# Performance work log

Measured on AMD Instinct MI355X. Metric: run time of the kernel, lower is better.

## Reference

```python
import jax, jax.numpy as jnp
import numpy as np

N = 100000      # nodes
E = 1600000     # edges (before self-loops)
IN = 256        # in_channels
HID = 16        # num_hid (per-head channels, layer 1)
HEADS = 4
OUT = 16        # out_channels (per-head channels, layer 2)
NEG_SLOPE = 0.2 # PyG GATConv default


def setup_inputs() -> dict:
    key = jax.random.key(0)
    ks = jax.random.split(key, 12)
    def glorot(k, shape, fan):
        return jax.random.normal(k, shape, jnp.float32) * (1.0 / np.sqrt(fan))
    x = jax.random.normal(ks[0], (N, IN), jnp.float32)
    edge_index = jax.random.randint(ks[1], (2, E), 0, N, dtype=jnp.int32)
    W1 = glorot(ks[2], (IN, HEADS * HID), IN)
    att_src1 = glorot(ks[3], (HEADS, HID), HID)
    att_dst1 = glorot(ks[4], (HEADS, HID), HID)
    b1 = jnp.zeros((HEADS * HID,), jnp.float32)
    W2 = glorot(ks[5], (HEADS * HID, HEADS * OUT), HEADS * HID)
    att_src2 = glorot(ks[6], (HEADS, OUT), OUT)
    att_dst2 = glorot(ks[7], (HEADS, OUT), OUT)
    b2 = jnp.zeros((HEADS * OUT,), jnp.float32)
    return {"x": x, "edge_index": edge_index, "W1": W1, "att_src1": att_src1,
            "att_dst1": att_dst1, "b1": b1, "W2": W2, "att_src2": att_src2,
            "att_dst2": att_dst2, "b2": b2}


def gat_conv(x, W, att_src, att_dst, bias, src, dst):
    # PyG GATConv (concat=True): h = xW per head; alpha via segment-softmax over dst.
    H, C = att_src.shape
    n = x.shape[0]
    h = (x @ W).reshape(n, H, C)                    # [N,H,C]
    a_s = jnp.sum(h * att_src, axis=-1)             # [N,H]
    a_d = jnp.sum(h * att_dst, axis=-1)             # [N,H]
    e = jax.nn.leaky_relu(a_s[src] + a_d[dst], NEG_SLOPE)  # [E',H]
    m = jax.lax.stop_gradient(jax.ops.segment_max(e, dst, num_segments=n))
    p = jnp.exp(e - m[dst])
    s = jax.ops.segment_sum(p, dst, num_segments=n)
    alpha = p / (s[dst] + 1e-16)                    # [E',H]
    msg = h[src] * alpha[:, :, None]                # [E',H,C] gathered messages
    out = jax.ops.segment_sum(msg, dst, num_segments=n)
    return out.reshape(n, H * C) + bias


def reference(x, edge_index, W1, att_src1, att_dst1, b1, W2, att_src2, att_dst2, b2):
    # add self loops (PyG GATConv default add_self_loops=True)
    loops = jnp.arange(N, dtype=edge_index.dtype)
    src = jnp.concatenate([edge_index[0], loops])
    dst = jnp.concatenate([edge_index[1], loops])
    h = jax.nn.relu(gat_conv(x, W1, att_src1, att_dst1, b1, src, dst))
    # dropout is identity in eval mode
    return gat_conv(h, W2, att_src2, att_dst2, b2, src, dst)
```

## Files before the change

### kernel.cpp

```cpp
#include <hip/hip_runtime.h>
#include <hip/hip_fp16.h>
#include <cstdint>


#define CH 4096
#define MAXB 512
#define SCAP 6144

using f16x8 = __attribute__((ext_vector_type(8))) _Float16;
using f32x4 = __attribute__((ext_vector_type(4))) float;

__device__ __forceinline__ float lrelu(float v) { return fmaxf(v, 0.2f * v); }

__global__ void ifill_kernel(int* __restrict__ p, int v, int n) {
  int i = blockIdx.x * blockDim.x + threadIdx.x;
  if (i < n) p[i] = v;
}

__global__ void wprep2_kernel(const float* __restrict__ W,
                              const float* __restrict__ as,
                              const float* __restrict__ ad,
                              ushort* __restrict__ WT, int K) {
  int i = blockIdx.x * 256 + threadIdx.x;
  if (i >= 80 * K) return;
  int c = i / K, k = i % K;
  float v = 0.f;
  if (c < 64) {
    v = W[k * 64 + c];
  } else if (c < 68) {
    int hd = c - 64;
    for (int j = 0; j < 16; ++j) v += W[k * 64 + hd * 16 + j] * as[hd * 16 + j];
  } else if (c < 72) {
    int hd = c - 68;
    for (int j = 0; j < 16; ++j) v += W[k * 64 + hd * 16 + j] * ad[hd * 16 + j];
  }
  WT[c * K + k] = __half_as_ushort(__float2half_rn(v));
}

__global__ __launch_bounds__(256) void bucket_hist(const int* __restrict__ edst,
                                                   int E, int nbuck,
                                                   int* __restrict__ bucket_cnt) {
  __shared__ int hist[MAXB];
  const int t = threadIdx.x;
  for (int j = t; j < MAXB; j += 256) hist[j] = 0;
  __syncthreads();
  const int base = blockIdx.x * CH;
#pragma unroll
  for (int k = 0; k < CH / 256; ++k) {
    int e = base + k * 256 + t;
    if (e < E) atomicAdd(&hist[edst[e] >> 8], 1);
  }
  __syncthreads();
  for (int j = t; j < nbuck; j += 256) {
    int c = hist[j];
    if (c) atomicAdd(&bucket_cnt[j], c);
  }
}

__global__ __launch_bounds__(512) void bucket_scan(const int* __restrict__ bucket_cnt,
                                                   int* __restrict__ bucket_base,
                                                   int* __restrict__ bucket_cursor,
                                                   int nbuck) {
  __shared__ int part[512];
  const int t = threadIdx.x;
  int v = (t < nbuck) ? bucket_cnt[t] : 0;
  part[t] = v;
  __syncthreads();
  for (int off = 1; off < 512; off <<= 1) {
    int u = (t >= off) ? part[t - off] : 0;
    __syncthreads();
    part[t] += u;
    __syncthreads();
  }
  int ex = part[t] - v;
  if (t <= nbuck) {
    int w = (t < nbuck) ? ex : part[nbuck - 1];
    bucket_base[t] = w;
    if (t < nbuck) bucket_cursor[t] = w;
  }
}

__global__ __launch_bounds__(256) void place_kernel(const int* __restrict__ esrc,
                                                    const int* __restrict__ edst,
                                                    int E, int nbuck,
                                                    int* __restrict__ bucket_cursor,
                                                    unsigned int* __restrict__ pairs) {
  __shared__ int hist[MAXB];
  __shared__ int gbase[MAXB];
  __shared__ int rcnt[MAXB];
  const int t = threadIdx.x;
  for (int j = t; j < MAXB; j += 256) { hist[j] = 0; rcnt[j] = 0; }
  __syncthreads();
  const int base = blockIdx.x * CH;
  int b_[CH / 256];
  unsigned int p_[CH / 256];
#pragma unroll
  for (int k = 0; k < CH / 256; ++k) {
    int e = base + k * 256 + t;
    if (e < E) {
      int d = edst[e];
      int s = esrc[e];
      b_[k] = d >> 8;
      p_[k] = ((unsigned int)s << 8) | (unsigned int)(d & 255);
      atomicAdd(&hist[b_[k]], 1);
    } else {
      b_[k] = -1;
    }
  }
  __syncthreads();
  for (int j = t; j < nbuck; j += 256) {
    int c = hist[j];
    gbase[j] = c ? atomicAdd(&bucket_cursor[j], c) : 0;
  }
  __syncthreads();
#pragma unroll
  for (int k = 0; k < CH / 256; ++k) {
    if (b_[k] >= 0) {
      int r = atomicAdd(&rcnt[b_[k]], 1);
      pairs[gbase[b_[k]] + r] = p_[k];
    }
  }
}

__global__ __launch_bounds__(256) void bucket_build(
    const unsigned int* __restrict__ pairs, const int* __restrict__ bucket_base,
    int* __restrict__ ccol, int* __restrict__ start, int* __restrict__ endp,
    int n) {
  __shared__ int cnt[256];
  __shared__ int ls[256];
  __shared__ int csave[256];
  __shared__ int part[256];
  __shared__ int sorted[SCAP];
  const int t = threadIdx.x;
  const int b = blockIdx.x;
  const int d0 = b << 8;
  const int DR = min(256, n - d0);
  const int in_base = bucket_base[b];
  const int nloc = bucket_base[b + 1] - in_base;
  const int out_base = in_base + d0;

  cnt[t] = (t < DR) ? 1 : 0;
  __syncthreads();
  for (int i = t; i < nloc; i += 256)
    atomicAdd(&cnt[pairs[in_base + i] & 255u], 1);
  __syncthreads();
  int c = cnt[t];
  csave[t] = c;
  part[t] = c;
  __syncthreads();
#pragma unroll
  for (int off = 1; off < 256; off <<= 1) {
    int u = (t >= off) ? part[t - off] : 0;
    __syncthreads();
    part[t] += u;
    __syncthreads();
  }
  ls[t] = part[t] - c;
  __syncthreads();
  if (t < DR) {
    int s = out_base + ls[t];
    start[d0 + t] = s;
    endp[d0 + t] = s + csave[t];
    sorted[ls[t]] = d0 + t;
    cnt[t] = 1;
  }
  __syncthreads();
  for (int i = t; i < nloc; i += 256) {
    unsigned int p = pairs[in_base + i];
    int j = (int)(p & 255u);
    int r = atomicAdd(&cnt[j], 1);
    int pos = ls[j] + r;
    if (pos < SCAP) sorted[pos] = (int)(p >> 8);
  }
  __syncthreads();
  int tot = nloc + DR;
  if (tot > SCAP) tot = SCAP;
  for (int i = t; i < tot; i += 256) ccol[out_base + i] = sorted[i];
}

template <int K, bool XHALF>
__global__ __launch_bounds__(256) void gemm_mfma(
    const void* __restrict__ xin, const ushort* __restrict__ wt,
    __half* __restrict__ h, float* __restrict__ as_, float* __restrict__ ad_,
    int n) {
  __shared__ _Float16 hs[64 * 88];
  __shared__ float att[64 * 12];
  const int tid = threadIdx.x;
  const int w = tid >> 6;
  const int lane = tid & 63;
  const int lr = lane & 15;
  const int kg = lane >> 4;
  const int row0 = blockIdx.x * 64;

  int rr = row0 + w * 16 + lr;
  if (rr > n - 1) rr = n - 1;

  constexpr int NS = K / 32;
  const ushort* wbase = wt + lr * K + kg * 8;

  f16x8 af[NS];
  if constexpr (!XHALF) {
    float4 av[NS][2];
    const float* xp = (const float*)xin + (long long)rr * K + kg * 8;
#pragma unroll
    for (int s = 0; s < NS; ++s) {
      av[s][0] = *(const float4*)(xp + s * 32);
      av[s][1] = *(const float4*)(xp + s * 32 + 4);
    }
#pragma unroll
    for (int s = 0; s < NS; ++s) {
      af[s][0] = (_Float16)av[s][0].x; af[s][1] = (_Float16)av[s][0].y;
      af[s][2] = (_Float16)av[s][0].z; af[s][3] = (_Float16)av[s][0].w;
      af[s][4] = (_Float16)av[s][1].x; af[s][5] = (_Float16)av[s][1].y;
      af[s][6] = (_Float16)av[s][1].z; af[s][7] = (_Float16)av[s][1].w;
    }
  } else {
    const ushort* xp = (const ushort*)xin + (long long)rr * K + kg * 8;
#pragma unroll
    for (int s = 0; s < NS; ++s)
      af[s] = *(const f16x8*)(xp + s * 32);
  }

  f32x4 acc[5] = {};
#pragma unroll
  for (int s = 0; s < NS; ++s) {
#pragma unroll
    for (int ct = 0; ct < 5; ++ct) {
      f16x8 b = *(const f16x8*)(wbase + ct * 16 * K + s * 32);
      acc[ct] = __builtin_amdgcn_mfma_f32_16x16x32_f16(af[s], b, acc[ct], 0, 0, 0);
    }
  }

  const int orow = w * 16 + kg * 4;
#pragma unroll
  for (int ct = 0; ct < 4; ++ct)
#pragma unroll
    for (int r = 0; r < 4; ++r)
      hs[(orow + r) * 88 + ct * 16 + lr] = (_Float16)acc[ct][r];
  if (lr < 8) {
#pragma unroll
    for (int r = 0; r < 4; ++r)
      att[(orow + r) * 12 + lr] = acc[4][r];
  }
  __syncthreads();

#pragma unroll
  for (int j = 0; j < 2; ++j) {
    int s = tid + j * 256;
    int row = s >> 3, seg = s & 7;
    if (row0 + row < n)
      *(uint4*)(h + (long long)(row0 + row) * 64 + seg * 8) =
          *(const uint4*)&hs[row * 88 + seg * 8];
  }
  if (tid < 64) {
    if (row0 + tid < n)
      *(float4*)(as_ + (long long)(row0 + tid) * 4) = *(const float4*)&att[tid * 12];
  } else if (tid < 128) {
    int t2 = tid - 64;
    if (row0 + t2 < n)
      *(float4*)(ad_ + (long long)(row0 + t2) * 4) = *(const float4*)&att[t2 * 12 + 4];
  }
}

__global__ __launch_bounds__(256) void node_agg_kernel(
    const int* __restrict__ ccol, const int* __restrict__ start,
    const int* __restrict__ endp,
    const float* __restrict__ as_, const float* __restrict__ ad_,
    const __half2* __restrict__ h2, const float* __restrict__ bias,
    float* __restrict__ fout, __half2* __restrict__ hout, int n, int mode) {
  const int node = blockIdx.x * 8 + (threadIdx.x >> 5);
  if (node >= n) return;
  const int hl = threadIdx.x & 31;
  const int hh = hl >> 3;
  const float adv = ad_[node * 4 + hh];
  const int s0i = start[node];
  const int d = endp[node] - s0i;
  const int* cp = ccol + s0i;
  float ax = 0.f, ay = 0.f, den = 0.f;
  int i = 0;
  for (; i + 4 <= d; i += 4) {
    int s0 = cp[i], s1 = cp[i + 1], s2 = cp[i + 2], s3 = cp[i + 3];
    float p0 = __expf(lrelu(as_[s0 * 4 + hh] + adv));
    float p1 = __expf(lrelu(as_[s1 * 4 + hh] + adv));
    float p2 = __expf(lrelu(as_[s2 * 4 + hh] + adv));
    float p3 = __expf(lrelu(as_[s3 * 4 + hh] + adv));
    float2 h0 = __half22float2(h2[s0 * 32 + hl]);
    float2 h1 = __half22float2(h2[s1 * 32 + hl]);
    float2 h2v = __half22float2(h2[s2 * 32 + hl]);
    float2 h3 = __half22float2(h2[s3 * 32 + hl]);
    den += (p0 + p1) + (p2 + p3);
    ax = fmaf(p0, h0.x, ax); ay = fmaf(p0, h0.y, ay);
    ax = fmaf(p1, h1.x, ax); ay = fmaf(p1, h1.y, ay);
    ax = fmaf(p2, h2v.x, ax); ay = fmaf(p2, h2v.y, ay);
    ax = fmaf(p3, h3.x, ax); ay = fmaf(p3, h3.y, ay);
  }
  for (; i < d; ++i) {
    int s0 = cp[i];
    float p0 = __expf(lrelu(as_[s0 * 4 + hh] + adv));
    float2 h0 = __half22float2(h2[s0 * 32 + hl]);
    den += p0;
    ax = fmaf(p0, h0.x, ax); ay = fmaf(p0, h0.y, ay);
  }
  const float inv = 1.0f / (den + 1e-16f);
  float vx = ax * inv + bias[hl * 2];
  float vy = ay * inv + bias[hl * 2 + 1];
  if (mode == 1) {
    vx = fmaxf(vx, 0.f);
    vy = fmaxf(vy, 0.f);
    hout[node * 32 + hl] = __floats2half2_rn(vx, vy);
  } else {
    *(float2*)(fout + node * 64 + hl * 2) = make_float2(vx, vy);
  }
}

extern "C" void kernel_launch(void* const* d_in, const int* in_sizes, int n_in,
                              void* d_out, int out_size, void* d_ws, size_t ws_size,
                              hipStream_t stream) {
  const float* x = (const float*)d_in[0];
  const int* ei = (const int*)d_in[1];
  const float* W1 = (const float*)d_in[2];
  const float* att_s1 = (const float*)d_in[3];
  const float* att_d1 = (const float*)d_in[4];
  const float* b1 = (const float*)d_in[5];
  const float* W2 = (const float*)d_in[6];
  const float* att_s2 = (const float*)d_in[7];
  const float* att_d2 = (const float*)d_in[8];
  const float* b2 = (const float*)d_in[9];

  const int n = in_sizes[0] / 256;
  const int E = in_sizes[1] / 2;
  const int* esrc = ei;
  const int* edst = ei + E;
  const int nbuck = (n + 255) >> 8;

  float* wsf = (float*)d_ws;
  __half* hbuf = (__half*)wsf;
  float* xbuf = wsf + (long long)n * 64;
  float* as_ = xbuf + (long long)n * 64;
  float* ad_ = as_ + (long long)n * 4;
  int* bucket_cnt = (int*)(ad_ + (long long)n * 4);
  int* bucket_base = bucket_cnt + MAXB;
  int* bucket_cursor = bucket_base + MAXB + 1;
  int* start = bucket_cursor + MAXB;
  int* endp = start + n;
  unsigned int* pairs = (unsigned int*)(endp + n);
  int* ccol = (int*)(pairs + E);
  ushort* wt1 = (ushort*)(((uintptr_t)(ccol + E + n) + 15) & ~(uintptr_t)15);
  ushort* wt2 = wt1 + 80 * 256;
  float* out = (float*)d_out;

  const int ebk = (E + CH - 1) / CH;
  const int gb = (n + 63) / 64;
  const int nb = (n + 7) / 8;

  wprep2_kernel<<<(80 * 256 + 255) / 256, 256, 0, stream>>>(W1, att_s1, att_d1, wt1, 256);
  wprep2_kernel<<<(80 * 64 + 255) / 256, 256, 0, stream>>>(W2, att_s2, att_d2, wt2, 64);

  ifill_kernel<<<(MAXB + 255) / 256, 256, 0, stream>>>(bucket_cnt, 0, MAXB);
  bucket_hist<<<ebk, 256, 0, stream>>>(edst, E, nbuck, bucket_cnt);
  bucket_scan<<<1, 512, 0, stream>>>(bucket_cnt, bucket_base, bucket_cursor, nbuck);
  place_kernel<<<ebk, 256, 0, stream>>>(esrc, edst, E, nbuck, bucket_cursor, pairs);
  bucket_build<<<nbuck, 256, 0, stream>>>(pairs, bucket_base, ccol, start, endp, n);

  gemm_mfma<256, false><<<gb, 256, 0, stream>>>(x, wt1, hbuf, as_, ad_, n);
  node_agg_kernel<<<nb, 256, 0, stream>>>(ccol, start, endp, as_, ad_,
                                          (const __half2*)hbuf, b1,
                                          nullptr, (__half2*)xbuf, n, 1);

  gemm_mfma<64, true><<<gb, 256, 0, stream>>>(xbuf, wt2, hbuf, as_, ad_, n);
  node_agg_kernel<<<nb, 256, 0, stream>>>(ccol, start, endp, as_, ad_,
                                          (const __half2*)hbuf, b2,
                                          out, nullptr, n, 0);
}
```

Before: 226.8 us.

## Fuse GEMM and aggregation stages into persistent kernel with grid barriers

Replaces the two GEMM and two aggregation launches with a single persistent kernel of 256 blocks that loops over tiles and node groups. The stages are separated by atomic-counter grid barriers, and the counters are zeroed by an extra fill launch. This removes inter-kernel launch gaps and tail effects. In exchange, the gather-heavy aggregation runs with far fewer resident blocks, which may reduce latency hiding, and the barrier relies on all blocks being co-resident.

```diff
diff --git a/kernel.cpp b/kernel.cpp
--- a/kernel.cpp
+++ b/kernel.cpp
@@ -6,6 +6,7 @@
 #define CH 4096
 #define MAXB 512
 #define SCAP 6144
+#define GRID_FUSED 256
 
 using f16x8 = __attribute__((ext_vector_type(8))) _Float16;
 using f32x4 = __attribute__((ext_vector_type(4))) float;
@@ -178,139 +179,176 @@
   for (int i = t; i < tot; i += 256) ccol[out_base + i] = sorted[i];
 }
 
+__device__ __forceinline__ void gsync(int* bar, int idx, int goal) {
+  __threadfence();
+  __syncthreads();
+  if (threadIdx.x == 0) {
+    atomicAdd(&bar[idx], 1);
+    while (atomicAdd(&bar[idx], 0) < goal) __builtin_amdgcn_s_sleep(2);
+  }
+  __syncthreads();
+  __threadfence();
+}
+
 template <int K, bool XHALF>
-__global__ __launch_bounds__(256) void gemm_mfma(
+__device__ __forceinline__ void gemm_phase(
     const void* __restrict__ xin, const ushort* __restrict__ wt,
     __half* __restrict__ h, float* __restrict__ as_, float* __restrict__ ad_,
-    int n) {
-  __shared__ _Float16 hs[64 * 88];
-  __shared__ float att[64 * 12];
+    int n, int ntiles, _Float16* hs, float* att) {
   const int tid = threadIdx.x;
   const int w = tid >> 6;
   const int lane = tid & 63;
   const int lr = lane & 15;
   const int kg = lane >> 4;
-  const int row0 = blockIdx.x * 64;
-
-  int rr = row0 + w * 16 + lr;
-  if (rr > n - 1) rr = n - 1;
-
   constexpr int NS = K / 32;
   const ushort* wbase = wt + lr * K + kg * 8;
 
-  f16x8 af[NS];
-  if constexpr (!XHALF) {
-    float4 av[NS][2];
-    const float* xp = (const float*)xin + (long long)rr * K + kg * 8;
-#pragma unroll
-    for (int s = 0; s < NS; ++s) {
-      av[s][0] = *(const float4*)(xp + s * 32);
-      av[s][1] = *(const float4*)(xp + s * 32 + 4);
-    }
-#pragma unroll
-    for (int s = 0; s < NS; ++s) {
-      af[s][0] = (_Float16)av[s][0].x; af[s][1] = (_Float16)av[s][0].y;
-      af[s][2] = (_Float16)av[s][0].z; af[s][3] = (_Float16)av[s][0].w;
-      af[s][4] = (_Float16)av[s][1].x; af[s][5] = (_Float16)av[s][1].y;
-      af[s][6] = (_Float16)av[s][1].z; af[s][7] = (_Float16)av[s][1].w;
-    }
-  } else {
-    const ushort* xp = (const ushort*)xin + (long long)rr * K + kg * 8;
+  for (int tile = blockIdx.x; tile < ntiles; tile += gridDim.x) {
+    const int row0 = tile * 64;
+    int rr = row0 + w * 16 + lr;
+    if (rr > n - 1) rr = n - 1;
+
+    f16x8 af[NS];
+    if constexpr (!XHALF) {
+      float4 av[NS][2];
+      const float* xp = (const float*)xin + (long long)rr * K + kg * 8;
+#pragma unroll
+      for (int s = 0; s < NS; ++s) {
+        av[s][0] = *(const float4*)(xp + s * 32);
+        av[s][1] = *(const float4*)(xp + s * 32 + 4);
+      }
+#pragma unroll
+      for (int s = 0; s < NS; ++s) {
+        af[s][0] = (_Float16)av[s][0].x; af[s][1] = (_Float16)av[s][0].y;
+        af[s][2] = (_Float16)av[s][0].z; af[s][3] = (_Float16)av[s][0].w;
+        af[s][4] = (_Float16)av[s][1].x; af[s][5] = (_Float16)av[s][1].y;
+        af[s][6] = (_Float16)av[s][1].z; af[s][7] = (_Float16)av[s][1].w;
+      }
+    } else {
+      const ushort* xp = (const ushort*)xin + (long long)rr * K + kg * 8;
+#pragma unroll
+      for (int s = 0; s < NS; ++s)
+        af[s] = *(const f16x8*)(xp + s * 32);
+    }
+
+    f32x4 acc[5] = {};
 #pragma unroll
     for (int s = 0; s < NS; ++s)
-      af[s] = *(const f16x8*)(xp + s * 32);
-  }
-
-  f32x4 acc[5] = {};
-#pragma unroll
-  for (int s = 0; s < NS; ++s) {
-#pragma unroll
-    for (int ct = 0; ct < 5; ++ct) {
-      f16x8 b = *(const f16x8*)(wbase + ct * 16 * K + s * 32);
-      acc[ct] = __builtin_amdgcn_mfma_f32_16x16x32_f16(af[s], b, acc[ct], 0, 0, 0);
-    }
-  }
-
-  const int orow = w * 16 + kg * 4;
-#pragma unroll
-  for (int ct = 0; ct < 4; ++ct)
-#pragma unroll
-    for (int r = 0; r < 4; ++r)
-      hs[(orow + r) * 88 + ct * 16 + lr] = (_Float16)acc[ct][r];
-  if (lr < 8) {
-#pragma unroll
-    for (int r = 0; r < 4; ++r)
-      att[(orow + r) * 12 + lr] = acc[4][r];
-  }
-  __syncthreads();
-
-#pragma unroll
-  for (int j = 0; j < 2; ++j) {
-    int s = tid + j * 256;
-    int row = s >> 3, seg = s & 7;
-    if (row0 + row < n)
-      *(uint4*)(h + (long long)(row0 + row) * 64 + seg * 8) =
-          *(const uint4*)&hs[row * 88 + seg * 8];
-  }
-  if (tid < 64) {
-    if (row0 + tid < n)
-      *(float4*)(as_ + (long long)(row0 + tid) * 4) = *(const float4*)&att[tid * 12];
-  } else if (tid < 128) {
-    int t2 = tid - 64;
-    if (row0 + t2 < n)
-      *(float4*)(ad_ + (long long)(row0 + t2) * 4) = *(const float4*)&att[t2 * 12 + 4];
-  }
-}
-
-__global__ __launch_bounds__(256) void node_agg_kernel(
+#pragma unroll
+      for (int ct = 0; ct < 5; ++ct) {
+        f16x8 b = *(const f16x8*)(wbase + ct * 16 * K + s * 32);
+        acc[ct] = __builtin_amdgcn_mfma_f32_16x16x32_f16(af[s], b, acc[ct], 0, 0, 0);
+      }
+
+    const int orow = w * 16 + kg * 4;
+#pragma unroll
+    for (int ct = 0; ct < 4; ++ct)
+#pragma unroll
+      for (int r = 0; r < 4; ++r)
+        hs[(orow + r) * 88 + ct * 16 + lr] = (_Float16)acc[ct][r];
+    if (lr < 8) {
+#pragma unroll
+      for (int r = 0; r < 4; ++r)
+        att[(orow + r) * 12 + lr] = acc[4][r];
+    }
+    __syncthreads();
+#pragma unroll
+    for (int j = 0; j < 2; ++j) {
+      int s = tid + j * 256;
+      int row = s >> 3, seg = s & 7;
+      if (row0 + row < n)
+        *(uint4*)(h + (long long)(row0 + row) * 64 + seg * 8) =
+            *(const uint4*)&hs[row * 88 + seg * 8];
+    }
+    if (tid < 64) {
+      if (row0 + tid < n)
+        *(float4*)(as_ + (long long)(row0 + tid) * 4) = *(const float4*)&att[tid * 12];
+    } else if (tid < 128) {
+      int t2 = tid - 64;
+      if (row0 + t2 < n)
+        *(float4*)(ad_ + (long long)(row0 + t2) * 4) = *(const float4*)&att[t2 * 12 + 4];
+    }
+    __syncthreads();
+  }
+}
+
+__device__ __forceinline__ void agg_phase(
     const int* __restrict__ ccol, const int* __restrict__ start,
     const int* __restrict__ endp,
     const float* __restrict__ as_, const float* __restrict__ ad_,
     const __half2* __restrict__ h2, const float* __restrict__ bias,
     float* __restrict__ fout, __half2* __restrict__ hout, int n, int mode) {
-  const int node = blockIdx.x * 8 + (threadIdx.x >> 5);
-  if (node >= n) return;
+  const int ngroups = (n + 7) / 8;
   const int hl = threadIdx.x & 31;
   const int hh = hl >> 3;
-  const float adv = ad_[node * 4 + hh];
-  const int s0i = start[node];
-  const int d = endp[node] - s0i;
-  const int* cp = ccol + s0i;
-  float ax = 0.f, ay = 0.f, den = 0.f;
-  int i = 0;
-  for (; i + 4 <= d; i += 4) {
-    int s0 = cp[i], s1 = cp[i + 1], s2 = cp[i + 2], s3 = cp[i + 3];
-    float p0 = __expf(lrelu(as_[s0 * 4 + hh] + adv));
-    float p1 = __expf(lrelu(as_[s1 * 4 + hh] + adv));
-    float p2 = __expf(lrelu(as_[s2 * 4 + hh] + adv));
-    float p3 = __expf(lrelu(as_[s3 * 4 + hh] + adv));
-    float2 h0 = __half22float2(h2[s0 * 32 + hl]);
-    float2 h1 = __half22float2(h2[s1 * 32 + hl]);
-    float2 h2v = __half22float2(h2[s2 * 32 + hl]);
-    float2 h3 = __half22float2(h2[s3 * 32 + hl]);
-    den += (p0 + p1) + (p2 + p3);
-    ax = fmaf(p0, h0.x, ax); ay = fmaf(p0, h0.y, ay);
-    ax = fmaf(p1, h1.x, ax); ay = fmaf(p1, h1.y, ay);
-    ax = fmaf(p2, h2v.x, ax); ay = fmaf(p2, h2v.y, ay);
-    ax = fmaf(p3, h3.x, ax); ay = fmaf(p3, h3.y, ay);
-  }
-  for (; i < d; ++i) {
-    int s0 = cp[i];
-    float p0 = __expf(lrelu(as_[s0 * 4 + hh] + adv));
-    float2 h0 = __half22float2(h2[s0 * 32 + hl]);
-    den += p0;
-    ax = fmaf(p0, h0.x, ax); ay = fmaf(p0, h0.y, ay);
-  }
-  const float inv = 1.0f / (den + 1e-16f);
-  float vx = ax * inv + bias[hl * 2];
-  float vy = ay * inv + bias[hl * 2 + 1];
-  if (mode == 1) {
-    vx = fmaxf(vx, 0.f);
-    vy = fmaxf(vy, 0.f);
-    hout[node * 32 + hl] = __floats2half2_rn(vx, vy);
-  } else {
-    *(float2*)(fout + node * 64 + hl * 2) = make_float2(vx, vy);
-  }
+  for (int g = blockIdx.x; g < ngroups; g += gridDim.x) {
+    const int node = g * 8 + (threadIdx.x >> 5);
+    if (node >= n) continue;
+    const float adv = ad_[node * 4 + hh];
+    const int s0i = start[node];
+    const int d = endp[node] - s0i;
+    const int* cp = ccol + s0i;
+    float ax = 0.f, ay = 0.f, den = 0.f;
+    int i = 0;
+    for (; i + 4 <= d; i += 4) {
+      int s0 = cp[i], s1 = cp[i + 1], s2 = cp[i + 2], s3 = cp[i + 3];
+      float p0 = __expf(lrelu(as_[s0 * 4 + hh] + adv));
+      float p1 = __expf(lrelu(as_[s1 * 4 + hh] + adv));
+      float p2 = __expf(lrelu(as_[s2 * 4 + hh] + adv));
+      float p3 = __expf(lrelu(as_[s3 * 4 + hh] + adv));
+      float2 h0 = __half22float2(h2[s0 * 32 + hl]);
+      float2 h1 = __half22float2(h2[s1 * 32 + hl]);
+      float2 h2v = __half22float2(h2[s2 * 32 + hl]);
+      float2 h3 = __half22float2(h2[s3 * 32 + hl]);
+      den += (p0 + p1) + (p2 + p3);
+      ax = fmaf(p0, h0.x, ax); ay = fmaf(p0, h0.y, ay);
+      ax = fmaf(p1, h1.x, ax); ay = fmaf(p1, h1.y, ay);
+      ax = fmaf(p2, h2v.x, ax); ay = fmaf(p2, h2v.y, ay);
+      ax = fmaf(p3, h3.x, ax); ay = fmaf(p3, h3.y, ay);
+    }
+    for (; i < d; ++i) {
+      int s0 = cp[i];
+      float p0 = __expf(lrelu(as_[s0 * 4 + hh] + adv));
+      float2 h0 = __half22float2(h2[s0 * 32 + hl]);
+      den += p0;
+      ax = fmaf(p0, h0.x, ax); ay = fmaf(p0, h0.y, ay);
+    }
+    const float inv = 1.0f / (den + 1e-16f);
+    float vx = ax * inv + bias[hl * 2];
+    float vy = ay * inv + bias[hl * 2 + 1];
+    if (mode == 1) {
+      vx = fmaxf(vx, 0.f);
+      vy = fmaxf(vy, 0.f);
+      hout[node * 32 + hl] = __floats2half2_rn(vx, vy);
+    } else {
+      *(float2*)(fout + node * 64 + hl * 2) = make_float2(vx, vy);
+    }
+  }
+}
+
+__global__ __launch_bounds__(256, 2) void fused_gat(
+    const float* __restrict__ x, const ushort* __restrict__ wt1,
+    const ushort* __restrict__ wt2,
+    const int* __restrict__ ccol, const int* __restrict__ start,
+    const int* __restrict__ endp,
+    const float* __restrict__ b1, const float* __restrict__ b2,
+    __half* __restrict__ hbuf, __half* __restrict__ xbuf_h,
+    float* __restrict__ as_, float* __restrict__ ad_, float* __restrict__ out,
+    int n, int* __restrict__ bar) {
+  __shared__ _Float16 hs[64 * 88];
+  __shared__ float att[64 * 12];
+  const int ntiles = (n + 63) >> 6;
+  const int goal = gridDim.x;
+
+  gemm_phase<256, false>(x, wt1, hbuf, as_, ad_, n, ntiles, hs, att);
+  gsync(bar, 0, goal);
+  agg_phase(ccol, start, endp, as_, ad_, (const __half2*)hbuf, b1,
+            nullptr, (__half2*)xbuf_h, n, 1);
+  gsync(bar, 1, goal);
+  gemm_phase<64, true>(xbuf_h, wt2, hbuf, as_, ad_, n, ntiles, hs, att);
+  gsync(bar, 2, goal);
+  agg_phase(ccol, start, endp, as_, ad_, (const __half2*)hbuf, b2,
+            out, nullptr, n, 0);
 }
 
 extern "C" void kernel_launch(void* const* d_in, const int* in_sizes, int n_in,
@@ -347,14 +385,14 @@
   int* ccol = (int*)(pairs + E);
   ushort* wt1 = (ushort*)(((uintptr_t)(ccol + E + n) + 15) & ~(uintptr_t)15);
   ushort* wt2 = wt1 + 80 * 256;
+  int* bar = (int*)(wt2 + 80 * 64);
   float* out = (float*)d_out;
 
   const int ebk = (E + CH - 1) / CH;
-  const int gb = (n + 63) / 64;
-  const int nb = (n + 7) / 8;
 
   wprep2_kernel<<<(80 * 256 + 255) / 256, 256, 0, stream>>>(W1, att_s1, att_d1, wt1, 256);
   wprep2_kernel<<<(80 * 64 + 255) / 256, 256, 0, stream>>>(W2, att_s2, att_d2, wt2, 64);
+  ifill_kernel<<<1, 256, 0, stream>>>(bar, 0, 4);
 
   ifill_kernel<<<(MAXB + 255) / 256, 256, 0, stream>>>(bucket_cnt, 0, MAXB);
   bucket_hist<<<ebk, 256, 0, stream>>>(edst, E, nbuck, bucket_cnt);
@@ -362,13 +400,7 @@
   place_kernel<<<ebk, 256, 0, stream>>>(esrc, edst, E, nbuck, bucket_cursor, pairs);
   bucket_build<<<nbuck, 256, 0, stream>>>(pairs, bucket_base, ccol, start, endp, n);
 
-  gemm_mfma<256, false><<<gb, 256, 0, stream>>>(x, wt1, hbuf, as_, ad_, n);
-  node_agg_kernel<<<nb, 256, 0, stream>>>(ccol, start, endp, as_, ad_,
-                                          (const __half2*)hbuf, b1,
-                                          nullptr, (__half2*)xbuf, n, 1);
-
-  gemm_mfma<64, true><<<gb, 256, 0, stream>>>(xbuf, wt2, hbuf, as_, ad_, n);
-  node_agg_kernel<<<nb, 256, 0, stream>>>(ccol, start, endp, as_, ad_,
-                                          (const __half2*)hbuf, b2,
-                                          out, nullptr, n, 0);
-}
+  fused_gat<<<GRID_FUSED, 256, 0, stream>>>(
+      x, wt1, wt2, ccol, start, endp, b1, b2,
+      hbuf, (__half*)xbuf, as_, ad_, out, n, bar);
+}
```

After: 709.5 us. +212.8%, slower.

## Fuse layer-2 linear transform and attention logits into layer-1 aggregation

Applied to the files above, without the earlier changes.

Replaces the second MFMA GEMM kernel and the W2 prep kernel by computing the 64x64 layer-2 projection per node inside the layer-1 aggregation kernel. It uses FP32 FMAs from shared memory and warp shuffles for the attention dot products. This removes the round trip of the intermediate activations through global memory and two kernel launches. In exchange the aggregation kernel does scalar FP32 matmul work per node, reads W2 from global/cache repeatedly, and adds a block-wide sync.

```diff
diff --git a/kernel.cpp b/kernel.cpp
--- a/kernel.cpp
+++ b/kernel.cpp
@@ -178,11 +178,11 @@
   for (int i = t; i < tot; i += 256) ccol[out_base + i] = sorted[i];
 }
 
-template <int K, bool XHALF>
-__global__ __launch_bounds__(256) void gemm_mfma(
-    const void* __restrict__ xin, const ushort* __restrict__ wt,
+__global__ __launch_bounds__(256) void gemm1_mfma(
+    const float* __restrict__ x, const ushort* __restrict__ wt,
     __half* __restrict__ h, float* __restrict__ as_, float* __restrict__ ad_,
     int n) {
+  constexpr int K = 256, NS = K / 32;
   __shared__ _Float16 hs[64 * 88];
   __shared__ float att[64 * 12];
   const int tid = threadIdx.x;
@@ -195,13 +195,12 @@
   int rr = row0 + w * 16 + lr;
   if (rr > n - 1) rr = n - 1;
 
-  constexpr int NS = K / 32;
   const ushort* wbase = wt + lr * K + kg * 8;
 
   f16x8 af[NS];
-  if constexpr (!XHALF) {
+  {
     float4 av[NS][2];
-    const float* xp = (const float*)xin + (long long)rr * K + kg * 8;
+    const float* xp = x + (long long)rr * K + kg * 8;
 #pragma unroll
     for (int s = 0; s < NS; ++s) {
       av[s][0] = *(const float4*)(xp + s * 32);
@@ -214,22 +213,16 @@
       af[s][4] = (_Float16)av[s][1].x; af[s][5] = (_Float16)av[s][1].y;
       af[s][6] = (_Float16)av[s][1].z; af[s][7] = (_Float16)av[s][1].w;
     }
-  } else {
-    const ushort* xp = (const ushort*)xin + (long long)rr * K + kg * 8;
-#pragma unroll
-    for (int s = 0; s < NS; ++s)
-      af[s] = *(const f16x8*)(xp + s * 32);
   }
 
   f32x4 acc[5] = {};
 #pragma unroll
-  for (int s = 0; s < NS; ++s) {
+  for (int s = 0; s < NS; ++s)
 #pragma unroll
     for (int ct = 0; ct < 5; ++ct) {
       f16x8 b = *(const f16x8*)(wbase + ct * 16 * K + s * 32);
       acc[ct] = __builtin_amdgcn_mfma_f32_16x16x32_f16(af[s], b, acc[ct], 0, 0, 0);
     }
-  }
 
   const int orow = w * 16 + kg * 4;
 #pragma unroll
@@ -243,7 +236,6 @@
       att[(orow + r) * 12 + lr] = acc[4][r];
   }
   __syncthreads();
-
 #pragma unroll
   for (int j = 0; j < 2; ++j) {
     int s = tid + j * 256;
@@ -262,17 +254,91 @@
   }
 }
 
-__global__ __launch_bounds__(256) void node_agg_kernel(
+__global__ __launch_bounds__(256) void agg1_kernel(
     const int* __restrict__ ccol, const int* __restrict__ start,
     const int* __restrict__ endp,
-    const float* __restrict__ as_, const float* __restrict__ ad_,
+    const float* __restrict__ as1, const float* __restrict__ ad1,
+    const __half2* __restrict__ h2in, const float* __restrict__ bias,
+    const float* __restrict__ W2, const float* __restrict__ a2s,
+    const float* __restrict__ a2d,
+    __half2* __restrict__ h2out, float* __restrict__ as2,
+    float* __restrict__ ad2, int n) {
+  __shared__ float x2s[8][65];
+  const int lw = threadIdx.x >> 5;
+  const int hl = threadIdx.x & 31;
+  const int hh = hl >> 3;
+  const int node = blockIdx.x * 8 + lw;
+  const bool act = node < n;
+  const int nodec = act ? node : 0;
+
+  const float adv = ad1[nodec * 4 + hh];
+  const int s0i = start[nodec];
+  const int d = act ? (endp[nodec] - s0i) : 0;
+  const int* cp = ccol + s0i;
+  float ax = 0.f, ay = 0.f, den = 0.f;
+  int i = 0;
+  for (; i + 4 <= d; i += 4) {
+    int s0 = cp[i], s1 = cp[i + 1], s2 = cp[i + 2], s3 = cp[i + 3];
+    float p0 = __expf(lrelu(as1[s0 * 4 + hh] + adv));
+    float p1 = __expf(lrelu(as1[s1 * 4 + hh] + adv));
+    float p2 = __expf(lrelu(as1[s2 * 4 + hh] + adv));
+    float p3 = __expf(lrelu(as1[s3 * 4 + hh] + adv));
+    float2 h0 = __half22float2(h2in[s0 * 32 + hl]);
+    float2 h1 = __half22float2(h2in[s1 * 32 + hl]);
+    float2 h2v = __half22float2(h2in[s2 * 32 + hl]);
+    float2 h3 = __half22float2(h2in[s3 * 32 + hl]);
+    den += (p0 + p1) + (p2 + p3);
+    ax = fmaf(p0, h0.x, ax); ay = fmaf(p0, h0.y, ay);
+    ax = fmaf(p1, h1.x, ax); ay = fmaf(p1, h1.y, ay);
+    ax = fmaf(p2, h2v.x, ax); ay = fmaf(p2, h2v.y, ay);
+    ax = fmaf(p3, h3.x, ax); ay = fmaf(p3, h3.y, ay);
+  }
+  for (; i < d; ++i) {
+    int s0 = cp[i];
+    float p0 = __expf(lrelu(as1[s0 * 4 + hh] + adv));
+    float2 h0 = __half22float2(h2in[s0 * 32 + hl]);
+    den += p0;
+    ax = fmaf(p0, h0.x, ax); ay = fmaf(p0, h0.y, ay);
+  }
+  const float inv = 1.0f / (den + 1e-16f);
+  float vx = act ? fmaxf(ax * inv + bias[hl * 2], 0.f) : 0.f;
+  float vy = act ? fmaxf(ay * inv + bias[hl * 2 + 1], 0.f) : 0.f;
+  x2s[lw][hl * 2] = vx;
+  x2s[lw][hl * 2 + 1] = vy;
+  __syncthreads();
+
+  float a0 = 0.f, a1 = 0.f;
+#pragma unroll 8
+  for (int k = 0; k < 64; ++k) {
+    float xk = x2s[lw][k];
+    float2 wv = *(const float2*)(W2 + k * 64 + hl * 2);
+    a0 = fmaf(xk, wv.x, a0);
+    a1 = fmaf(xk, wv.y, a1);
+  }
+  if (act) h2out[node * 32 + hl] = __floats2half2_rn(a0, a1);
+
+  const int j0 = (hl * 2) & 15;
+  float ps = a0 * a2s[hh * 16 + j0] + a1 * a2s[hh * 16 + j0 + 1];
+  float pd = a0 * a2d[hh * 16 + j0] + a1 * a2d[hh * 16 + j0 + 1];
+  ps += __shfl_xor(ps, 1); ps += __shfl_xor(ps, 2); ps += __shfl_xor(ps, 4);
+  pd += __shfl_xor(pd, 1); pd += __shfl_xor(pd, 2); pd += __shfl_xor(pd, 4);
+  if ((hl & 7) == 0 && act) {
+    as2[node * 4 + hh] = ps;
+    ad2[node * 4 + hh] = pd;
+  }
+}
+
+__global__ __launch_bounds__(256) void agg2_kernel(
+    const int* __restrict__ ccol, const int* __restrict__ start,
+    const int* __restrict__ endp,
+    const float* __restrict__ as2, const float* __restrict__ ad2,
     const __half2* __restrict__ h2, const float* __restrict__ bias,
-    float* __restrict__ fout, __half2* __restrict__ hout, int n, int mode) {
+    float* __restrict__ out, int n) {
   const int node = blockIdx.x * 8 + (threadIdx.x >> 5);
   if (node >= n) return;
   const int hl = threadIdx.x & 31;
   const int hh = hl >> 3;
-  const float adv = ad_[node * 4 + hh];
+  const float adv = ad2[node * 4 + hh];
   const int s0i = start[node];
   const int d = endp[node] - s0i;
   const int* cp = ccol + s0i;
@@ -280,10 +346,10 @@
   int i = 0;
   for (; i + 4 <= d; i += 4) {
     int s0 = cp[i], s1 = cp[i + 1], s2 = cp[i + 2], s3 = cp[i + 3];
-    float p0 = __expf(lrelu(as_[s0 * 4 + hh] + adv));
-    float p1 = __expf(lrelu(as_[s1 * 4 + hh] + adv));
-    float p2 = __expf(lrelu(as_[s2 * 4 + hh] + adv));
-    float p3 = __expf(lrelu(as_[s3 * 4 + hh] + adv));
+    float p0 = __expf(lrelu(as2[s0 * 4 + hh] + adv));
+    float p1 = __expf(lrelu(as2[s1 * 4 + hh] + adv));
+    float p2 = __expf(lrelu(as2[s2 * 4 + hh] + adv));
+    float p3 = __expf(lrelu(as2[s3 * 4 + hh] + adv));
     float2 h0 = __half22float2(h2[s0 * 32 + hl]);
     float2 h1 = __half22float2(h2[s1 * 32 + hl]);
     float2 h2v = __half22float2(h2[s2 * 32 + hl]);
@@ -296,7 +362,7 @@
   }
   for (; i < d; ++i) {
     int s0 = cp[i];
-    float p0 = __expf(lrelu(as_[s0 * 4 + hh] + adv));
+    float p0 = __expf(lrelu(as2[s0 * 4 + hh] + adv));
     float2 h0 = __half22float2(h2[s0 * 32 + hl]);
     den += p0;
     ax = fmaf(p0, h0.x, ax); ay = fmaf(p0, h0.y, ay);
@@ -304,13 +370,7 @@
   const float inv = 1.0f / (den + 1e-16f);
   float vx = ax * inv + bias[hl * 2];
   float vy = ay * inv + bias[hl * 2 + 1];
-  if (mode == 1) {
-    vx = fmaxf(vx, 0.f);
-    vy = fmaxf(vy, 0.f);
-    hout[node * 32 + hl] = __floats2half2_rn(vx, vy);
-  } else {
-    *(float2*)(fout + node * 64 + hl * 2) = make_float2(vx, vy);
-  }
+  *(float2*)(out + (long long)node * 64 + hl * 2) = make_float2(vx, vy);
 }
 
 extern "C" void kernel_launch(void* const* d_in, const int* in_sizes, int n_in,
@@ -335,10 +395,12 @@
 
   float* wsf = (float*)d_ws;
   __half* hbuf = (__half*)wsf;
-  float* xbuf = wsf + (long long)n * 64;
-  float* as_ = xbuf + (long long)n * 64;
-  float* ad_ = as_ + (long long)n * 4;
-  int* bucket_cnt = (int*)(ad_ + (long long)n * 4);
+  __half* h2buf = (__half*)(wsf + (long long)n * 32);
+  float* as1 = wsf + (long long)n * 64;
+  float* ad1 = as1 + (long long)n * 4;
+  float* as2 = ad1 + (long long)n * 4;
+  float* ad2 = as2 + (long long)n * 4;
+  int* bucket_cnt = (int*)(ad2 + (long long)n * 4);
   int* bucket_base = bucket_cnt + MAXB;
   int* bucket_cursor = bucket_base + MAXB + 1;
   int* start = bucket_cursor + MAXB;
@@ -346,15 +408,13 @@
   unsigned int* pairs = (unsigned int*)(endp + n);
   int* ccol = (int*)(pairs + E);
   ushort* wt1 = (ushort*)(((uintptr_t)(ccol + E + n) + 15) & ~(uintptr_t)15);
-  ushort* wt2 = wt1 + 80 * 256;
   float* out = (float*)d_out;
 
   const int ebk = (E + CH - 1) / CH;
   const int gb = (n + 63) / 64;
-  const int nb = (n + 7) / 8;
+  const int nb1 = (n + 7) / 8;
 
   wprep2_kernel<<<(80 * 256 + 255) / 256, 256, 0, stream>>>(W1, att_s1, att_d1, wt1, 256);
-  wprep2_kernel<<<(80 * 64 + 255) / 256, 256, 0, stream>>>(W2, att_s2, att_d2, wt2, 64);
 
   ifill_kernel<<<(MAXB + 255) / 256, 256, 0, stream>>>(bucket_cnt, 0, MAXB);
   bucket_hist<<<ebk, 256, 0, stream>>>(edst, E, nbuck, bucket_cnt);
@@ -362,13 +422,12 @@
   place_kernel<<<ebk, 256, 0, stream>>>(esrc, edst, E, nbuck, bucket_cursor, pairs);
   bucket_build<<<nbuck, 256, 0, stream>>>(pairs, bucket_base, ccol, start, endp, n);
 
-  gemm_mfma<256, false><<<gb, 256, 0, stream>>>(x, wt1, hbuf, as_, ad_, n);
-  node_agg_kernel<<<nb, 256, 0, stream>>>(ccol, start, endp, as_, ad_,
-                                          (const __half2*)hbuf, b1,
-                                          nullptr, (__half2*)xbuf, n, 1);
-
-  gemm_mfma<64, true><<<gb, 256, 0, stream>>>(xbuf, wt2, hbuf, as_, ad_, n);
-  node_agg_kernel<<<nb, 256, 0, stream>>>(ccol, start, endp, as_, ad_,
-                                          (const __half2*)hbuf, b2,
-                                          out, nullptr, n, 0);
-}
+  gemm1_mfma<<<gb, 256, 0, stream>>>(x, wt1, hbuf, as1, ad1, n);
+  agg1_kernel<<<nb1, 256, 0, stream>>>(ccol, start, endp, as1, ad1,
+                                       (const __half2*)hbuf, b1,
+                                       W2, att_s2, att_d2,
+                                       (__half2*)h2buf, as2, ad2, n);
+
+  agg2_kernel<<<nb1, 256, 0, stream>>>(ccol, start, endp, as2, ad2,
+                                       (const __half2*)h2buf, b2, out, n);
+}
```

New measurement: 284.6 us. 1.25x slower.
